# Kernel optimization log

Measured on AMD Instinct MI355X. Metric: run time of the kernel, lower is better.

The kernel has to match this reference:

```python
import jax, jax.numpy as jnp
import numpy as np

VOCAB = 32000
HID = 1024
IN_DIM = 768
LAYERS = 2


def setup_inputs() -> dict:
    key = jax.random.key(0)
    ks = jax.random.split(key, 12)
    s = 0.02
    B, N, S = 8, 16, 512
    return {
        "concepts": jax.random.normal(ks[0], (B, N, IN_DIM), dtype=jnp.float32),
        "target_sequence": jax.random.randint(ks[1], (B, S), 0, VOCAB),
        "embedding": s * jax.random.normal(ks[2], (VOCAB, HID), dtype=jnp.float32),
        "w_ih": s * jax.random.normal(ks[3], (LAYERS, 3 * HID, HID), dtype=jnp.float32),
        "w_hh": s * jax.random.normal(ks[4], (LAYERS, 3 * HID, HID), dtype=jnp.float32),
        "b_ih": jnp.zeros((LAYERS, 3 * HID), dtype=jnp.float32),
        "b_hh": jnp.zeros((LAYERS, 3 * HID), dtype=jnp.float32),
        "fc_w": s * jax.random.normal(ks[5], (VOCAB, HID), dtype=jnp.float32),
        "fc_b": jnp.zeros((VOCAB,), dtype=jnp.float32),
        "c2h_w": s * jax.random.normal(ks[6], (HID * LAYERS, IN_DIM), dtype=jnp.float32),
        "c2h_b": jnp.zeros((HID * LAYERS,), dtype=jnp.float32),
    }


def _gru_layer(x, h0, w_ih, w_hh, b_ih, b_hh):
    # x: [B,S,H], h0: [B,H]. PyTorch GRU gate order: r, z, n.
    xg = jnp.einsum('bsh,gh->bsg', x, w_ih) + b_ih  # precompute input gates [B,S,3H]

    def step(h, xg_t):
        hg = h @ w_hh.T + b_hh
        xr, xz, xn = jnp.split(xg_t, 3, axis=-1)
        hr, hz, hn = jnp.split(hg, 3, axis=-1)
        r = jax.nn.sigmoid(xr + hr)
        z = jax.nn.sigmoid(xz + hz)
        n = jnp.tanh(xn + r * hn)
        h_new = (1.0 - z) * n + z * h
        return h_new, h_new

    _, ys = jax.lax.scan(step, h0, jnp.swapaxes(xg, 0, 1))  # [S,B,H]
    return jnp.swapaxes(ys, 0, 1)


def reference(concepts, target_sequence, embedding, w_ih, w_hh, b_ih, b_hh,
              fc_w, fc_b, c2h_w, c2h_b):
    B = concepts.shape[0]
    global_context = jnp.mean(concepts, axis=1)  # [B, D]
    h0 = (global_context @ c2h_w.T + c2h_b).reshape(B, LAYERS, HID)
    h0 = jnp.swapaxes(h0, 0, 1)  # [L, B, H] matching torch view(L, B, H)
    x = embedding[target_sequence]  # [B, S, H]
    for l in range(LAYERS):
        x = _gru_layer(x, h0[l], w_ih[l], w_hh[l], b_ih[l], b_hh[l])
    logits = jnp.einsum('bsh,vh->bsv', x, fc_w) + fc_b
    return logits
```

## Files before the change

### kernel.cpp

```cpp
#include <hip/hip_runtime.h>
#include <hip/hip_bf16.h>
#include <stdint.h>

#define B_ 8
#define S_ 512
#define H_ 1024
#define V_ 32000
#define D_ 768
#define G3H (3*H_)

typedef __bf16 bf16x8_t __attribute__((ext_vector_type(8)));
typedef float f32x4_t __attribute__((ext_vector_type(4)));

__device__ __forceinline__ unsigned short f2bf(float f) {
  unsigned int u = __float_as_uint(f);
  u += 0x7fffu + ((u >> 16) & 1u);
  return (unsigned short)(u >> 16);
}
__device__ __forceinline__ float fast_sigmoid(float x) {
  float e = __builtin_amdgcn_exp2f(x * -1.44269504088896340736f);
  return __builtin_amdgcn_rcpf(1.0f + e);
}
__device__ __forceinline__ float fast_tanh(float x) {
  float e = __builtin_amdgcn_exp2f(x * -2.88539008177792681472f);
  return 2.0f * __builtin_amdgcn_rcpf(1.0f + e) - 1.0f;
}

__global__ void zero_buf(uint4* __restrict__ p, int n) {
  int i = blockIdx.x * 256 + threadIdx.x;
  if (i < n) p[i] = uint4{0, 0, 0, 0};
}

__global__ void ctx_mean(const float* __restrict__ c, float* __restrict__ ctx) {
  int b = blockIdx.x;
  for (int d = threadIdx.x; d < D_; d += 256) {
    float s = 0.f;
    #pragma unroll
    for (int n = 0; n < 16; ++n) s += c[((size_t)b * 16 + n) * D_ + d];
    ctx[b * D_ + d] = s * (1.0f / 16.0f);
  }
}

__global__ void h0_compute(const float* __restrict__ ctx, const float* __restrict__ w,
                           const float* __restrict__ bias, float* __restrict__ h0l,
                           unsigned short* __restrict__ hb) {
  int o = blockIdx.x * 256 + threadIdx.x;
  int b = o >> 11, row = o & 2047;
  float s = bias[row];
  const float* cw = w + (size_t)row * D_;
  const float* cb = ctx + b * D_;
  for (int d = 0; d < D_; ++d) s += cb[d] * cw[d];
  int layer = row >> 10, u = row & 1023;
  h0l[((size_t)layer * 8 + b) * 1024 + u] = s;
  hb[(size_t)layer * 32768 + b * 1024 + u] = f2bf(s);
}

__global__ void gather_embed(const int* __restrict__ seq, const float* __restrict__ emb,
                             unsigned short* __restrict__ x) {
  int r = blockIdx.x;
  int idx = seq[r];
  float4 v = ((const float4*)(emb + (size_t)idx * H_))[threadIdx.x];
  ushort4 o;
  o.x = f2bf(v.x); o.y = f2bf(v.y); o.z = f2bf(v.z); o.w = f2bf(v.w);
  ((ushort4*)(x + (size_t)r * H_))[threadIdx.x] = o;
}

__global__ void f32_to_bf16(const float* __restrict__ in, unsigned short* __restrict__ outp, long n4) {
  long i = blockIdx.x * (long)blockDim.x + threadIdx.x;
  long stride = (long)gridDim.x * blockDim.x;
  for (; i < n4; i += stride) {
    float4 v = ((const float4*)in)[i];
    ushort4 o;
    o.x = f2bf(v.x); o.y = f2bf(v.y); o.z = f2bf(v.z); o.w = f2bf(v.w);
    ((ushort4*)outp)[i] = o;
  }
}

__global__ __launch_bounds__(256) void gemm_bt_bf16(
    const unsigned short* __restrict__ A, const unsigned short* __restrict__ B,
    float* __restrict__ C, const float* __restrict__ bias,
    int M, int N, int K)
{
  __shared__ __align__(16) unsigned short As[128 * 32];
  __shared__ __align__(16) unsigned short Bs[128 * 32];
  const int tid = threadIdx.x;
  const int l = tid & 63;
  const int w = tid >> 6;
  const int wr = w >> 1, wc = w & 1;
  const long row0 = (long)blockIdx.y * 128;
  const long col0 = (long)blockIdx.x * 128;

  f32x4_t acc[4][4];
  #pragma unroll
  for (int m = 0; m < 4; ++m)
    #pragma unroll
    for (int n = 0; n < 4; ++n) acc[m][n] = (f32x4_t)0.0f;

  const int sr = tid >> 2;
  const int sc = (tid & 3) << 3;

  for (int kt = 0; kt < K; kt += 32) {
    __syncthreads();
    uint4 a0 = *(const uint4*)&A[(row0 + sr) * K + kt + sc];
    uint4 a1 = *(const uint4*)&A[(row0 + sr + 64) * K + kt + sc];
    uint4 b0 = *(const uint4*)&B[(col0 + sr) * K + kt + sc];
    uint4 b1 = *(const uint4*)&B[(col0 + sr + 64) * K + kt + sc];
    ((uint4*)As)[tid]       = a0;
    ((uint4*)As)[tid + 256] = a1;
    ((uint4*)Bs)[tid]       = b0;
    ((uint4*)Bs)[tid + 256] = b1;
    __syncthreads();

    bf16x8_t af[4], bfr[4];
    #pragma unroll
    for (int m = 0; m < 4; ++m)
      af[m] = *(const bf16x8_t*)&As[(wr * 64 + m * 16 + (l & 15)) * 32 + (l >> 4) * 8];
    #pragma unroll
    for (int n = 0; n < 4; ++n)
      bfr[n] = *(const bf16x8_t*)&Bs[(wc * 64 + n * 16 + (l & 15)) * 32 + (l >> 4) * 8];
    #pragma unroll
    for (int m = 0; m < 4; ++m)
      #pragma unroll
      for (int n = 0; n < 4; ++n)
        acc[m][n] = __builtin_amdgcn_mfma_f32_16x16x32_bf16(af[m], bfr[n], acc[m][n], 0, 0, 0);
  }

  #pragma unroll
  for (int n = 0; n < 4; ++n) {
    const long col = col0 + wc * 64 + n * 16 + (l & 15);
    const float bv = bias[col];
    #pragma unroll
    for (int m = 0; m < 4; ++m) {
      const long rbase = row0 + wr * 64 + m * 16 + ((l >> 4) << 2);
      #pragma unroll
      for (int v = 0; v < 4; ++v)
        C[(rbase + v) * (long)N + col] = acc[m][n][v] + bv;
    }
  }
}

__device__ __forceinline__ void load_wfrag(const float* __restrict__ W, int j0, int w,
                                           int l15, int lhi, bf16x8_t wf[2][8]) {
  #pragma unroll
  for (int m = 0; m < 2; ++m) {
    const int idx = m * 16 + l15;
    const int gg = idx >> 3, uu = idx & 7;
    #pragma unroll
    for (int c = 0; c < 8; ++c) {
      f32x4_t v0 = {0.f, 0.f, 0.f, 0.f}, v1 = {0.f, 0.f, 0.f, 0.f};
      if (idx < 24) {
        const float* p = W + (size_t)((gg << 10) + j0 + uu) * 1024
                           + (w << 8) + (c << 5) + (lhi << 3);
        v0 = *(const f32x4_t*)p;
        v1 = *(const f32x4_t*)(p + 4);
      }
      bf16x8_t f;
      f[0] = (__bf16)v0[0]; f[1] = (__bf16)v0[1]; f[2] = (__bf16)v0[2]; f[3] = (__bf16)v0[3];
      f[4] = (__bf16)v1[0]; f[5] = (__bf16)v1[1]; f[6] = (__bf16)v1[2]; f[7] = (__bf16)v1[3];
      wf[m][c] = f;
    }
  }
}

__global__ __launch_bounds__(256, 1) void gru_fused(
    const float* __restrict__ xg,
    const float* __restrict__ w_hh,
    const float* __restrict__ w_ih,
    const float* __restrict__ b_hh,
    const float* __restrict__ b_ih,
    const float* __restrict__ h0f,
    unsigned short* __restrict__ y,
    unsigned short* __restrict__ hb,
    int* __restrict__ flags)
{
  __shared__ __align__(16) float red[4 * 3 * 256];
  const int tid = threadIdx.x;
  const int blk = blockIdx.x;
  const int layer = blk >> 7;
  const int j0 = (blk & 127) * 8;
  const int w = tid >> 6;
  const int l = tid & 63;
  const int l15 = l & 15;
  const int lhi = l >> 4;

  const float* whh = w_hh + (size_t)layer * G3H * H_;
  const float* bhh = b_hh + (size_t)layer * G3H;
  const float* bih = b_ih + (size_t)layer * G3H;

  bf16x8_t wfh[2][8], wfi[2][8];
  #pragma unroll
  for (int m = 0; m < 2; ++m)
    #pragma unroll
    for (int c = 0; c < 8; ++c) wfi[m][c] = (bf16x8_t)(__bf16)0.0f;
  load_wfrag(whh, j0, w, l15, lhi, wfh);
  if (layer == 1) load_wfrag(w_ih + (size_t)G3H * H_, j0, w, l15, lhi, wfi);

  const int u = tid & 7;
  const int b = tid >> 3;
  float g_br = 0.f, g_bz = 0.f, g_bnh = 0.f, g_bni = 0.f, hprev = 0.f;
  const float* xgp = nullptr;
  if (tid < 64) {
    float bhr = bhh[j0 + u], bhz = bhh[1024 + j0 + u], bhn = bhh[2048 + j0 + u];
    if (layer == 0) {
      g_br = bhr; g_bz = bhz; g_bnh = bhn;
      xgp = xg + (size_t)(b * S_) * G3H + j0 + u;
    } else {
      g_br = bhr + bih[j0 + u];
      g_bz = bhz + bih[1024 + j0 + u];
      g_bnh = bhn;
      g_bni = bih[2048 + j0 + u];
    }
    hprev = h0f[(size_t)layer * 8192 + b * 1024 + j0 + u];
  }

  unsigned short* const hb0 = hb;
  unsigned short* const hb1 = hb + 32768;
  const int frag_off = l15 * 1024 + (w << 8) + (lhi << 3);

  for (int e = 0; e <= S_; ++e) {
    const bool active = (layer == 0) ? (e < S_) : (e >= 1);
    const int t = (layer == 0) ? e : (e - 1);

    f32x4_t hv[8], yv[8];
    #pragma unroll
    for (int c = 0; c < 8; ++c) { hv[c] = (f32x4_t)0.0f; yv[c] = (f32x4_t)0.0f; }
    float xr = 0.f, xz = 0.f, xn = 0.f;

    f32x4_t a0h = (f32x4_t)0.0f, a1h = (f32x4_t)0.0f, a1i = (f32x4_t)0.0f;

    if (active) {
      if (layer == 0) {
        const unsigned short* hp0 = hb0 + (e & 1) * 16384 + frag_off;
        #pragma unroll
        for (int c = 0; c < 8; ++c)
          asm volatile("global_load_dwordx4 %0, %1, off offset:%2 sc0 sc1"
                       : "=v"(hv[c]) : "v"(hp0), "i"(c * 64) : "memory");
        if (tid < 64) {
          const float* p = xgp + (size_t)t * G3H;
          xr = p[0]; xz = p[1024]; xn = p[2048];
        }
      } else {
        const unsigned short* yp0 = hb0 + (e & 1) * 16384 + frag_off;
        const unsigned short* hp0 = hb1 + ((e + 1) & 1) * 16384 + frag_off;
        #pragma unroll
        for (int c = 0; c < 8; ++c)
          asm volatile("global_load_dwordx4 %0, %1, off offset:%2 sc0 sc1"
                       : "=v"(yv[c]) : "v"(yp0), "i"(c * 64) : "memory");
        #pragma unroll
        for (int c = 0; c < 8; ++c)
          asm volatile("global_load_dwordx4 %0, %1, off offset:%2 sc0 sc1"
                       : "=v"(hv[c]) : "v"(hp0), "i"(c * 64) : "memory");
      }
      asm volatile("s_waitcnt vmcnt(0)" ::: "memory");
      __builtin_amdgcn_sched_barrier(0);

      #pragma unroll
      for (int c = 0; c < 8; ++c) {
        bf16x8_t hfc = __builtin_bit_cast(bf16x8_t, hv[c]);
        a0h = __builtin_amdgcn_mfma_f32_16x16x32_bf16(wfh[0][c], hfc, a0h, 0, 0, 0);
        a1h = __builtin_amdgcn_mfma_f32_16x16x32_bf16(wfh[1][c], hfc, a1h, 0, 0, 0);
      }
      if (layer == 1) {
        #pragma unroll
        for (int c = 0; c < 8; ++c) {
          bf16x8_t yfc = __builtin_bit_cast(bf16x8_t, yv[c]);
          a0h = __builtin_amdgcn_mfma_f32_16x16x32_bf16(wfi[0][c], yfc, a0h, 0, 0, 0);
          a1i = __builtin_amdgcn_mfma_f32_16x16x32_bf16(wfi[1][c], yfc, a1i, 0, 0, 0);
        }
      }
      *(f32x4_t*)&red[(w * 3 + 0) * 256 + (l << 2)] = a0h;
      *(f32x4_t*)&red[(w * 3 + 1) * 256 + (l << 2)] = a1h;
      *(f32x4_t*)&red[(w * 3 + 2) * 256 + (l << 2)] = a1i;
    }
    __syncthreads();

    if (active && tid < 64) {
      const int base0 = (((u >> 2) << 4 | b) << 2) + (u & 3);
      const int base1 = base0 + 128;
      float aR = 0.f, aZ = 0.f, aNh = 0.f, aNi = 0.f;
      #pragma unroll
      for (int ww = 0; ww < 4; ++ww) {
        aR  += red[ww * 768 + base0];
        aZ  += red[ww * 768 + base1];
        aNh += red[ww * 768 + 256 + base0];
        aNi += red[ww * 768 + 512 + base0];
      }
      float r, z, n;
      if (layer == 0) {
        r = fast_sigmoid(xr + g_br + aR);
        z = fast_sigmoid(xz + g_bz + aZ);
        n = fast_tanh(xn + r * (aNh + g_bnh));
      } else {
        r = fast_sigmoid(aR + g_br);
        z = fast_sigmoid(aZ + g_bz);
        n = fast_tanh(aNi + g_bni + r * (aNh + g_bnh));
      }
      hprev = (1.0f - z) * n + z * hprev;
      unsigned short hv16 = f2bf(hprev);
      unsigned short* hdst = (layer == 0) ? (hb0 + ((e + 1) & 1) * 16384)
                                          : (hb1 + (e & 1) * 16384);
      if (layer == 1)
        y[(((size_t)(b * S_ + t)) << 10) + j0 + u] = hv16;
      asm volatile("global_store_short %0, %1, off sc0 sc1"
                   :: "v"(hdst + b * 1024 + j0 + u), "v"(hv16) : "memory");
    }
    asm volatile("s_waitcnt vmcnt(0)" ::: "memory");
    __syncthreads();
    if (tid == 0)
      __hip_atomic_store(&flags[blk * 32], e + 1,
                         __ATOMIC_RELAXED, __HIP_MEMORY_SCOPE_AGENT);
    while (__hip_atomic_load(&flags[tid * 32],
                             __ATOMIC_RELAXED, __HIP_MEMORY_SCOPE_AGENT) < e + 1)
      __builtin_amdgcn_s_sleep(1);
    __syncthreads();
  }
}

extern "C" void kernel_launch(void* const* d_in, const int* in_sizes, int n_in,
                              void* d_out, int out_size, void* d_ws, size_t ws_size,
                              hipStream_t stream) {
  (void)in_sizes; (void)n_in; (void)out_size; (void)ws_size;
  const float* concepts = (const float*)d_in[0];
  const int*   seq      = (const int*)d_in[1];
  const float* emb      = (const float*)d_in[2];
  const float* w_ih     = (const float*)d_in[3];
  const float* w_hh     = (const float*)d_in[4];
  const float* b_ih     = (const float*)d_in[5];
  const float* b_hh     = (const float*)d_in[6];
  const float* fc_w     = (const float*)d_in[7];
  const float* fc_b     = (const float*)d_in[8];
  const float* c2h_w    = (const float*)d_in[9];
  const float* c2h_b    = (const float*)d_in[10];
  float* out = (float*)d_out;

  char* ws = (char*)d_ws;
  size_t off = 0;
  auto alloc = [&](size_t bytes) {
    char* p = ws + off;
    off += (bytes + 255) & ~(size_t)255;
    return p;
  };
  unsigned short* xy   = (unsigned short*)alloc((size_t)B_ * S_ * H_ * 2);
  float*          xg   = (float*)alloc((size_t)B_ * S_ * G3H * 4);
  unsigned short* wihb = (unsigned short*)alloc((size_t)G3H * H_ * 2);
  unsigned short* fcwb = (unsigned short*)alloc((size_t)V_ * H_ * 2);
  float*          ctx  = (float*)alloc((size_t)B_ * D_ * 4);
  float*          h0l  = (float*)alloc((size_t)2 * B_ * H_ * 4);
  unsigned short* hb   = (unsigned short*)alloc((size_t)2 * 2 * 16 * 1024 * 2);
  int*            flags= (int*)alloc((size_t)256 * 32 * 4);

  zero_buf<<<dim3(40), dim3(256), 0, stream>>>((uint4*)hb, (131072 + 32768) / 16);
  ctx_mean<<<dim3(8), dim3(256), 0, stream>>>(concepts, ctx);
  h0_compute<<<dim3(64), dim3(256), 0, stream>>>(ctx, c2h_w, c2h_b, h0l, hb);
  gather_embed<<<dim3(B_ * S_), dim3(256), 0, stream>>>(seq, emb, xy);
  f32_to_bf16<<<dim3(1024), dim3(256), 0, stream>>>(w_ih, wihb, (long)G3H * H_ / 4);
  f32_to_bf16<<<dim3(2048), dim3(256), 0, stream>>>(fc_w, fcwb, (long)V_ * H_ / 4);

  gemm_bt_bf16<<<dim3(G3H / 128, (B_ * S_) / 128), dim3(256), 0, stream>>>(
      xy, wihb, xg, b_ih, B_ * S_, G3H, H_);

  gru_fused<<<dim3(256), dim3(256), 0, stream>>>(
      xg, w_hh, w_ih, b_hh, b_ih, h0l, xy, hb, flags);

  gemm_bt_bf16<<<dim3(V_ / 128, (B_ * S_) / 128), dim3(256), 0, stream>>>(
      xy, fcwb, out, fc_b, B_ * S_, V_, H_);
}
```

Before: 2.703 ms.

## Replace global barrier with tagged hidden-state words and per-layer ack flags

The per-step grid-wide flag barrier is removed from the fused GRU kernel. Each hidden-state value is now stored as a 32-bit word carrying the bf16 value and a step tag, and consumers poll their own fragments until every tag matches the expected step. Layer 0 waits only on per-block acks from layer 1 before it overwrites the double-buffered state. This cuts the all-to-all barrier latency on the sequential critical path, at the cost of twice the state traffic, spin-polling loads, and added complexity in the memory-ordering logic.

Result: slower. 4.762 ms (+76.2%).

```diff
diff --git a/kernel.cpp b/kernel.cpp
--- a/kernel.cpp
+++ b/kernel.cpp
@@ -43,7 +43,7 @@
 
 __global__ void h0_compute(const float* __restrict__ ctx, const float* __restrict__ w,
                            const float* __restrict__ bias, float* __restrict__ h0l,
-                           unsigned short* __restrict__ hb) {
+                           uint32_t* __restrict__ tagw) {
   int o = blockIdx.x * 256 + threadIdx.x;
   int b = o >> 11, row = o & 2047;
   float s = bias[row];
@@ -52,7 +52,8 @@
   for (int d = 0; d < D_; ++d) s += cb[d] * cw[d];
   int layer = row >> 10, u = row & 1023;
   h0l[((size_t)layer * 8 + b) * 1024 + u] = s;
-  hb[(size_t)layer * 32768 + b * 1024 + u] = f2bf(s);
+  uint32_t tag = (layer == 0) ? 0u : 1u;
+  tagw[(size_t)layer * 16384 + b * 1024 + u] = (tag << 16) | (uint32_t)f2bf(s);
 }
 
 __global__ void gather_embed(const int* __restrict__ seq, const float* __restrict__ emb,
@@ -139,6 +140,53 @@
   }
 }
 
+template<int NCH>
+__device__ __forceinline__ void poll_tagged(const uint32_t* b0, const uint32_t* b1,
+                                            uint32_t tag, uint4 (&q0)[NCH], uint4 (&q1)[NCH]) {
+  #pragma unroll
+  for (int c = 0; c < NCH; ++c) {
+    const uint32_t* p = (c < 8) ? (b0 + c * 32) : (b1 + (c - 8) * 32);
+    asm volatile("global_load_dwordx4 %0, %2, off sc0 sc1\n\t"
+                 "global_load_dwordx4 %1, %2, off offset:16 sc0 sc1"
+                 : "=&v"(q0[c]), "=&v"(q1[c]) : "v"(p) : "memory");
+  }
+  asm volatile("s_waitcnt vmcnt(0)" ::: "memory");
+  while (true) {
+    uint32_t bad = 0;
+    bool st[NCH];
+    #pragma unroll
+    for (int c = 0; c < NCH; ++c) {
+      uint32_t m = (q0[c].x >> 16) ^ tag;
+      m |= (q0[c].y >> 16) ^ tag;  m |= (q0[c].z >> 16) ^ tag;  m |= (q0[c].w >> 16) ^ tag;
+      m |= (q1[c].x >> 16) ^ tag;  m |= (q1[c].y >> 16) ^ tag;
+      m |= (q1[c].z >> 16) ^ tag;  m |= (q1[c].w >> 16) ^ tag;
+      st[c] = (m != 0);
+      bad |= m;
+    }
+    if (bad == 0) break;
+    __builtin_amdgcn_s_sleep(1);
+    #pragma unroll
+    for (int c = 0; c < NCH; ++c) {
+      if (st[c]) {
+        const uint32_t* p = (c < 8) ? (b0 + c * 32) : (b1 + (c - 8) * 32);
+        asm volatile("global_load_dwordx4 %0, %2, off sc0 sc1\n\t"
+                     "global_load_dwordx4 %1, %2, off offset:16 sc0 sc1"
+                     : "=&v"(q0[c]), "=&v"(q1[c]) : "v"(p) : "memory");
+      }
+    }
+    asm volatile("s_waitcnt vmcnt(0)" ::: "memory");
+  }
+}
+
+__device__ __forceinline__ bf16x8_t pack8(const uint4 a, const uint4 b) {
+  uint4 r;
+  r.x = (a.x & 0xFFFFu) | (a.y << 16);
+  r.y = (a.z & 0xFFFFu) | (a.w << 16);
+  r.z = (b.x & 0xFFFFu) | (b.y << 16);
+  r.w = (b.z & 0xFFFFu) | (b.w << 16);
+  return __builtin_bit_cast(bf16x8_t, r);
+}
+
 __device__ __forceinline__ void load_wfrag(const float* __restrict__ W, int j0, int w,
                                            int l15, int lhi, bf16x8_t wf[2][8]) {
   #pragma unroll
@@ -170,8 +218,8 @@
     const float* __restrict__ b_ih,
     const float* __restrict__ h0f,
     unsigned short* __restrict__ y,
-    unsigned short* __restrict__ hb,
-    int* __restrict__ flags)
+    uint32_t* __restrict__ tagw,
+    int* __restrict__ acks)
 {
   __shared__ __align__(16) float red[4 * 3 * 256];
   const int tid = threadIdx.x;
@@ -182,6 +230,7 @@
   const int l = tid & 63;
   const int l15 = l & 15;
   const int lhi = l >> 4;
+  const bool realrow = (l15 < 8);
 
   const float* whh = w_hh + (size_t)layer * G3H * H_;
   const float* bhh = b_hh + (size_t)layer * G3H;
@@ -213,59 +262,63 @@
     hprev = h0f[(size_t)layer * 8192 + b * 1024 + j0 + u];
   }
 
-  unsigned short* const hb0 = hb;
-  unsigned short* const hb1 = hb + 32768;
-  const int frag_off = l15 * 1024 + (w << 8) + (lhi << 3);
+  uint32_t* const tb0 = tagw;
+  uint32_t* const tb1 = tagw + 16384;
+  const int frag_u32 = l15 * 1024 + (w << 8) + (lhi << 3);
+
+  __syncthreads();
 
   for (int e = 0; e <= S_; ++e) {
     const bool active = (layer == 0) ? (e < S_) : (e >= 1);
     const int t = (layer == 0) ? e : (e - 1);
-
-    f32x4_t hv[8], yv[8];
-    #pragma unroll
-    for (int c = 0; c < 8; ++c) { hv[c] = (f32x4_t)0.0f; yv[c] = (f32x4_t)0.0f; }
+    const uint32_t tag = (uint32_t)e;
+
+    if (layer == 0 && active && tid < 128) {
+      while (__hip_atomic_load(&acks[tid], __ATOMIC_RELAXED, __HIP_MEMORY_SCOPE_AGENT) < e - 1)
+        __builtin_amdgcn_s_sleep(1);
+    }
+
     float xr = 0.f, xz = 0.f, xn = 0.f;
-
     f32x4_t a0h = (f32x4_t)0.0f, a1h = (f32x4_t)0.0f, a1i = (f32x4_t)0.0f;
 
     if (active) {
       if (layer == 0) {
-        const unsigned short* hp0 = hb0 + (e & 1) * 16384 + frag_off;
-        #pragma unroll
-        for (int c = 0; c < 8; ++c)
-          asm volatile("global_load_dwordx4 %0, %1, off offset:%2 sc0 sc1"
-                       : "=v"(hv[c]) : "v"(hp0), "i"(c * 64) : "memory");
         if (tid < 64) {
           const float* p = xgp + (size_t)t * G3H;
           xr = p[0]; xz = p[1024]; xn = p[2048];
         }
-      } else {
-        const unsigned short* yp0 = hb0 + (e & 1) * 16384 + frag_off;
-        const unsigned short* hp0 = hb1 + ((e + 1) & 1) * 16384 + frag_off;
+        uint4 q0[8], q1[8];
         #pragma unroll
-        for (int c = 0; c < 8; ++c)
-          asm volatile("global_load_dwordx4 %0, %1, off offset:%2 sc0 sc1"
-                       : "=v"(yv[c]) : "v"(yp0), "i"(c * 64) : "memory");
-        #pragma unroll
-        for (int c = 0; c < 8; ++c)
-          asm volatile("global_load_dwordx4 %0, %1, off offset:%2 sc0 sc1"
-                       : "=v"(hv[c]) : "v"(hp0), "i"(c * 64) : "memory");
-      }
-      asm volatile("s_waitcnt vmcnt(0)" ::: "memory");
-      __builtin_amdgcn_sched_barrier(0);
-
-      #pragma unroll
-      for (int c = 0; c < 8; ++c) {
-        bf16x8_t hfc = __builtin_bit_cast(bf16x8_t, hv[c]);
-        a0h = __builtin_amdgcn_mfma_f32_16x16x32_bf16(wfh[0][c], hfc, a0h, 0, 0, 0);
-        a1h = __builtin_amdgcn_mfma_f32_16x16x32_bf16(wfh[1][c], hfc, a1h, 0, 0, 0);
-      }
-      if (layer == 1) {
+        for (int c = 0; c < 8; ++c) { q0[c] = uint4{0,0,0,0}; q1[c] = uint4{0,0,0,0}; }
+        if (realrow) {
+          const uint32_t* hp = tb0 + (e & 1) * 8192 + frag_u32;
+          poll_tagged<8>(hp, hp, tag, q0, q1);
+        }
+        __builtin_amdgcn_sched_barrier(0);
         #pragma unroll
         for (int c = 0; c < 8; ++c) {
-          bf16x8_t yfc = __builtin_bit_cast(bf16x8_t, yv[c]);
-          a0h = __builtin_amdgcn_mfma_f32_16x16x32_bf16(wfi[0][c], yfc, a0h, 0, 0, 0);
-          a1i = __builtin_amdgcn_mfma_f32_16x16x32_bf16(wfi[1][c], yfc, a1i, 0, 0, 0);
+          bf16x8_t hf = pack8(q0[c], q1[c]);
+          a0h = __builtin_amdgcn_mfma_f32_16x16x32_bf16(wfh[0][c], hf, a0h, 0, 0, 0);
+          a1h = __builtin_amdgcn_mfma_f32_16x16x32_bf16(wfh[1][c], hf, a1h, 0, 0, 0);
+        }
+      } else {
+        uint4 q0[16], q1[16];
+        #pragma unroll
+        for (int c = 0; c < 16; ++c) { q0[c] = uint4{0,0,0,0}; q1[c] = uint4{0,0,0,0}; }
+        if (realrow) {
+          const uint32_t* yp = tb0 + (e & 1) * 8192 + frag_u32;
+          const uint32_t* hp = tb1 + ((e + 1) & 1) * 8192 + frag_u32;
+          poll_tagged<16>(yp, hp, tag, q0, q1);
+        }
+        __builtin_amdgcn_sched_barrier(0);
+        #pragma unroll
+        for (int c = 0; c < 8; ++c) {
+          bf16x8_t yf = pack8(q0[c], q1[c]);
+          bf16x8_t hf = pack8(q0[8 + c], q1[8 + c]);
+          a0h = __builtin_amdgcn_mfma_f32_16x16x32_bf16(wfh[0][c], hf, a0h, 0, 0, 0);
+          a1h = __builtin_amdgcn_mfma_f32_16x16x32_bf16(wfh[1][c], hf, a1h, 0, 0, 0);
+          a0h = __builtin_amdgcn_mfma_f32_16x16x32_bf16(wfi[0][c], yf, a0h, 0, 0, 0);
+          a1i = __builtin_amdgcn_mfma_f32_16x16x32_bf16(wfi[1][c], yf, a1i, 0, 0, 0);
         }
       }
       *(f32x4_t*)&red[(w * 3 + 0) * 256 + (l << 2)] = a0h;
@@ -273,6 +326,9 @@
       *(f32x4_t*)&red[(w * 3 + 2) * 256 + (l << 2)] = a1i;
     }
     __syncthreads();
+
+    if (layer == 1 && active && tid == 0)
+      __hip_atomic_store(&acks[blk & 127], e, __ATOMIC_RELAXED, __HIP_MEMORY_SCOPE_AGENT);
 
     if (active && tid < 64) {
       const int base0 = (((u >> 2) << 4 | b) << 2) + (u & 3);
@@ -297,21 +353,15 @@
       }
       hprev = (1.0f - z) * n + z * hprev;
       unsigned short hv16 = f2bf(hprev);
-      unsigned short* hdst = (layer == 0) ? (hb0 + ((e + 1) & 1) * 16384)
-                                          : (hb1 + (e & 1) * 16384);
+      uint32_t word = ((uint32_t)(e + 1) << 16) | (uint32_t)hv16;
+      uint32_t* hdst = (layer == 0)
+          ? (tb0 + ((e + 1) & 1) * 8192 + b * 1024 + j0 + u)
+          : (tb1 + (e & 1) * 8192 + b * 1024 + j0 + u);
       if (layer == 1)
         y[(((size_t)(b * S_ + t)) << 10) + j0 + u] = hv16;
-      asm volatile("global_store_short %0, %1, off sc0 sc1"
-                   :: "v"(hdst + b * 1024 + j0 + u), "v"(hv16) : "memory");
-    }
-    asm volatile("s_waitcnt vmcnt(0)" ::: "memory");
-    __syncthreads();
-    if (tid == 0)
-      __hip_atomic_store(&flags[blk * 32], e + 1,
-                         __ATOMIC_RELAXED, __HIP_MEMORY_SCOPE_AGENT);
-    while (__hip_atomic_load(&flags[tid * 32],
-                             __ATOMIC_RELAXED, __HIP_MEMORY_SCOPE_AGENT) < e + 1)
-      __builtin_amdgcn_s_sleep(1);
+      asm volatile("global_store_dword %0, %1, off sc0 sc1"
+                   :: "v"(hdst), "v"(word) : "memory");
+    }
     __syncthreads();
   }
 }
@@ -346,12 +396,12 @@
   unsigned short* fcwb = (unsigned short*)alloc((size_t)V_ * H_ * 2);
   float*          ctx  = (float*)alloc((size_t)B_ * D_ * 4);
   float*          h0l  = (float*)alloc((size_t)2 * B_ * H_ * 4);
-  unsigned short* hb   = (unsigned short*)alloc((size_t)2 * 2 * 16 * 1024 * 2);
-  int*            flags= (int*)alloc((size_t)256 * 32 * 4);
-
-  zero_buf<<<dim3(40), dim3(256), 0, stream>>>((uint4*)hb, (131072 + 32768) / 16);
+  uint32_t*       tagw = (uint32_t*)alloc((size_t)2 * 2 * 8 * 1024 * 4);
+  int*            acks = (int*)alloc((size_t)128 * 4);
+
+  zero_buf<<<dim3(1), dim3(256), 0, stream>>>((uint4*)acks, 128 / 4);
   ctx_mean<<<dim3(8), dim3(256), 0, stream>>>(concepts, ctx);
-  h0_compute<<<dim3(64), dim3(256), 0, stream>>>(ctx, c2h_w, c2h_b, h0l, hb);
+  h0_compute<<<dim3(64), dim3(256), 0, stream>>>(ctx, c2h_w, c2h_b, h0l, tagw);
   gather_embed<<<dim3(B_ * S_), dim3(256), 0, stream>>>(seq, emb, xy);
   f32_to_bf16<<<dim3(1024), dim3(256), 0, stream>>>(w_ih, wihb, (long)G3H * H_ / 4);
   f32_to_bf16<<<dim3(2048), dim3(256), 0, stream>>>(fc_w, fcwb, (long)V_ * H_ / 4);
@@ -360,7 +410,7 @@
       xy, wihb, xg, b_ih, B_ * S_, G3H, H_);
 
   gru_fused<<<dim3(256), dim3(256), 0, stream>>>(
-      xg, w_hh, w_ih, b_hh, b_ih, h0l, xy, hb, flags);
+      xg, w_hh, w_ih, b_hh, b_ih, h0l, xy, tagw, acks);
 
   gemm_bt_bf16<<<dim3(V_ / 128, (B_ * S_) / 128), dim3(256), 0, stream>>>(
       xy, fcwb, out, fc_b, B_ * S_, V_, H_);
```

## Halve GRU persistent blocks and replace global barrier with targeted flag waits

Applied to the files above, without the earlier changes.

The persistent GRU kernel now runs on 128 blocks, each owning 16 hidden units with three gate MFMA fragments per wave, instead of 256 blocks with 8 units. The all-to-all barrier at the end of every step is replaced by waits at the start of each step on only the producer flags it depends on. Layer 0 gets a triple-buffered hidden state so it can run one step ahead of layer 1. Hidden-state stores are widened to packed dwords. The aim is to cut per-step barrier latency, at the cost of more register pressure and more MFMA work per block.

New measurement: 2.505 ms. -7.3%, faster.

```diff
diff --git a/kernel.cpp b/kernel.cpp
--- a/kernel.cpp
+++ b/kernel.cpp
@@ -52,7 +52,7 @@
   for (int d = 0; d < D_; ++d) s += cb[d] * cw[d];
   int layer = row >> 10, u = row & 1023;
   h0l[((size_t)layer * 8 + b) * 1024 + u] = s;
-  hb[(size_t)layer * 32768 + b * 1024 + u] = f2bf(s);
+  hb[(layer ? 24576 : 0) + b * 1024 + u] = f2bf(s);
 }
 
 __global__ void gather_embed(const int* __restrict__ seq, const float* __restrict__ emb,
@@ -139,21 +139,15 @@
   }
 }
 
-__device__ __forceinline__ void load_wfrag(const float* __restrict__ W, int j0, int w,
-                                           int l15, int lhi, bf16x8_t wf[2][8]) {
+__device__ __forceinline__ void load_wfrag3(const float* __restrict__ W, int j0, int w,
+                                            int l15, int lhi, bf16x8_t wf[3][8]) {
   #pragma unroll
-  for (int m = 0; m < 2; ++m) {
-    const int idx = m * 16 + l15;
-    const int gg = idx >> 3, uu = idx & 7;
+  for (int m = 0; m < 3; ++m) {
+    const float* pr = W + (size_t)((m << 10) + j0 + l15) * 1024 + (w << 8) + (lhi << 3);
     #pragma unroll
     for (int c = 0; c < 8; ++c) {
-      f32x4_t v0 = {0.f, 0.f, 0.f, 0.f}, v1 = {0.f, 0.f, 0.f, 0.f};
-      if (idx < 24) {
-        const float* p = W + (size_t)((gg << 10) + j0 + uu) * 1024
-                           + (w << 8) + (c << 5) + (lhi << 3);
-        v0 = *(const f32x4_t*)p;
-        v1 = *(const f32x4_t*)(p + 4);
-      }
+      f32x4_t v0 = *(const f32x4_t*)(pr + (c << 5));
+      f32x4_t v1 = *(const f32x4_t*)(pr + (c << 5) + 4);
       bf16x8_t f;
       f[0] = (__bf16)v0[0]; f[1] = (__bf16)v0[1]; f[2] = (__bf16)v0[2]; f[3] = (__bf16)v0[3];
       f[4] = (__bf16)v1[0]; f[5] = (__bf16)v1[1]; f[6] = (__bf16)v1[2]; f[7] = (__bf16)v1[3];
@@ -171,148 +165,169 @@
     const float* __restrict__ h0f,
     unsigned short* __restrict__ y,
     unsigned short* __restrict__ hb,
-    int* __restrict__ flags)
+    int* __restrict__ fl)
 {
-  __shared__ __align__(16) float red[4 * 3 * 256];
+  __shared__ __align__(16) float red[4 * 4 * 256];
   const int tid = threadIdx.x;
   const int blk = blockIdx.x;
-  const int layer = blk >> 7;
-  const int j0 = (blk & 127) * 8;
+  const int layer = blk >> 6;
+  const int j0 = (blk & 63) << 4;
   const int w = tid >> 6;
   const int l = tid & 63;
   const int l15 = l & 15;
   const int lhi = l >> 4;
-
-  const float* whh = w_hh + (size_t)layer * G3H * H_;
-  const float* bhh = b_hh + (size_t)layer * G3H;
-  const float* bih = b_ih + (size_t)layer * G3H;
-
-  bf16x8_t wfh[2][8], wfi[2][8];
+  const bool realrow = (l15 < 8);
+
+  bf16x8_t wfh[3][8], wfi[3][8];
   #pragma unroll
-  for (int m = 0; m < 2; ++m)
+  for (int m = 0; m < 3; ++m)
     #pragma unroll
     for (int c = 0; c < 8; ++c) wfi[m][c] = (bf16x8_t)(__bf16)0.0f;
-  load_wfrag(whh, j0, w, l15, lhi, wfh);
-  if (layer == 1) load_wfrag(w_ih + (size_t)G3H * H_, j0, w, l15, lhi, wfi);
-
-  const int u = tid & 7;
+  load_wfrag3(w_hh + (size_t)layer * G3H * H_, j0, w, l15, lhi, wfh);
+  if (layer == 1) load_wfrag3(w_ih + (size_t)G3H * H_, j0, w, l15, lhi, wfi);
+
+  const int up = tid & 7;
   const int b = tid >> 3;
-  float g_br = 0.f, g_bz = 0.f, g_bnh = 0.f, g_bni = 0.f, hprev = 0.f;
+  float gbr0 = 0.f, gbz0 = 0.f, gbnh0 = 0.f, gbni0 = 0.f, hp0 = 0.f;
+  float gbr1 = 0.f, gbz1 = 0.f, gbnh1 = 0.f, gbni1 = 0.f, hp1 = 0.f;
   const float* xgp = nullptr;
   if (tid < 64) {
-    float bhr = bhh[j0 + u], bhz = bhh[1024 + j0 + u], bhn = bhh[2048 + j0 + u];
+    const float* bhh_l = b_hh + (size_t)layer * G3H;
+    const float* bih_l = b_ih + (size_t)layer * G3H;
+    const int uj = j0 + 2 * up;
+    float bhr0 = bhh_l[uj],     bhz0 = bhh_l[1024 + uj],     bhn0 = bhh_l[2048 + uj];
+    float bhr1 = bhh_l[uj + 1], bhz1 = bhh_l[1024 + uj + 1], bhn1 = bhh_l[2048 + uj + 1];
     if (layer == 0) {
-      g_br = bhr; g_bz = bhz; g_bnh = bhn;
-      xgp = xg + (size_t)(b * S_) * G3H + j0 + u;
+      gbr0 = bhr0; gbz0 = bhz0; gbnh0 = bhn0;
+      gbr1 = bhr1; gbz1 = bhz1; gbnh1 = bhn1;
+      xgp = xg + (size_t)(b * S_) * G3H + uj;
     } else {
-      g_br = bhr + bih[j0 + u];
-      g_bz = bhz + bih[1024 + j0 + u];
-      g_bnh = bhn;
-      g_bni = bih[2048 + j0 + u];
-    }
-    hprev = h0f[(size_t)layer * 8192 + b * 1024 + j0 + u];
+      gbr0 = bhr0 + bih_l[uj];     gbz0 = bhz0 + bih_l[1024 + uj];
+      gbnh0 = bhn0;                gbni0 = bih_l[2048 + uj];
+      gbr1 = bhr1 + bih_l[uj + 1]; gbz1 = bhz1 + bih_l[1024 + uj + 1];
+      gbnh1 = bhn1;                gbni1 = bih_l[2048 + uj + 1];
+    }
+    float2 h2 = *(const float2*)&h0f[(size_t)layer * 8192 + b * 1024 + uj];
+    hp0 = h2.x; hp1 = h2.y;
   }
 
   unsigned short* const hb0 = hb;
-  unsigned short* const hb1 = hb + 32768;
-  const int frag_off = l15 * 1024 + (w << 8) + (lhi << 3);
+  unsigned short* const hb1 = hb + 24576;
+  const int frag = l15 * 1024 + (w << 8) + (lhi << 3);
 
   for (int e = 0; e <= S_; ++e) {
     const bool active = (layer == 0) ? (e < S_) : (e >= 1);
     const int t = (layer == 0) ? e : (e - 1);
-
-    f32x4_t hv[8], yv[8];
-    #pragma unroll
-    for (int c = 0; c < 8; ++c) { hv[c] = (f32x4_t)0.0f; yv[c] = (f32x4_t)0.0f; }
-    float xr = 0.f, xz = 0.f, xn = 0.f;
-
-    f32x4_t a0h = (f32x4_t)0.0f, a1h = (f32x4_t)0.0f, a1i = (f32x4_t)0.0f;
+    const int s3 = e % 3;
+
+    if (tid >= 64 && tid < 192) {
+      const int idx = tid - 64;
+      const int thr = (idx < 64) ? e : ((layer == 0) ? (e - 1) : e);
+      while (__hip_atomic_load(&fl[idx * 32], __ATOMIC_RELAXED, __HIP_MEMORY_SCOPE_AGENT) < thr)
+        __builtin_amdgcn_s_sleep(1);
+    }
+    __syncthreads();
+
+    f32x4_t accR = (f32x4_t)0.0f, accZ = (f32x4_t)0.0f;
+    f32x4_t accNh = (f32x4_t)0.0f, accNi = (f32x4_t)0.0f;
+    float2 xr2 = {0.f, 0.f}, xz2 = {0.f, 0.f}, xn2 = {0.f, 0.f};
 
     if (active) {
-      if (layer == 0) {
-        const unsigned short* hp0 = hb0 + (e & 1) * 16384 + frag_off;
+      f32x4_t hv[8], yv[8];
+      #pragma unroll
+      for (int c = 0; c < 8; ++c) { hv[c] = (f32x4_t)0.0f; yv[c] = (f32x4_t)0.0f; }
+      if (realrow) {
+        const unsigned short* hp = (layer == 0) ? (hb0 + s3 * 8192 + frag)
+                                                : (hb1 + ((e + 1) & 1) * 8192 + frag);
         #pragma unroll
         for (int c = 0; c < 8; ++c)
           asm volatile("global_load_dwordx4 %0, %1, off offset:%2 sc0 sc1"
-                       : "=v"(hv[c]) : "v"(hp0), "i"(c * 64) : "memory");
-        if (tid < 64) {
-          const float* p = xgp + (size_t)t * G3H;
-          xr = p[0]; xz = p[1024]; xn = p[2048];
+                       : "=v"(hv[c]) : "v"(hp), "i"(c * 64) : "memory");
+        if (layer == 1) {
+          const unsigned short* yp = hb0 + s3 * 8192 + frag;
+          #pragma unroll
+          for (int c = 0; c < 8; ++c)
+            asm volatile("global_load_dwordx4 %0, %1, off offset:%2 sc0 sc1"
+                         : "=v"(yv[c]) : "v"(yp), "i"(c * 64) : "memory");
         }
-      } else {
-        const unsigned short* yp0 = hb0 + (e & 1) * 16384 + frag_off;
-        const unsigned short* hp0 = hb1 + ((e + 1) & 1) * 16384 + frag_off;
-        #pragma unroll
-        for (int c = 0; c < 8; ++c)
-          asm volatile("global_load_dwordx4 %0, %1, off offset:%2 sc0 sc1"
-                       : "=v"(yv[c]) : "v"(yp0), "i"(c * 64) : "memory");
-        #pragma unroll
-        for (int c = 0; c < 8; ++c)
-          asm volatile("global_load_dwordx4 %0, %1, off offset:%2 sc0 sc1"
-                       : "=v"(hv[c]) : "v"(hp0), "i"(c * 64) : "memory");
+      }
+      if (layer == 0 && tid < 64) {
+        const float* p = xgp + (size_t)t * G3H;
+        xr2 = *(const float2*)p;
+        xz2 = *(const float2*)(p + 1024);
+        xn2 = *(const float2*)(p + 2048);
       }
       asm volatile("s_waitcnt vmcnt(0)" ::: "memory");
       __builtin_amdgcn_sched_barrier(0);
 
       #pragma unroll
       for (int c = 0; c < 8; ++c) {
-        bf16x8_t hfc = __builtin_bit_cast(bf16x8_t, hv[c]);
-        a0h = __builtin_amdgcn_mfma_f32_16x16x32_bf16(wfh[0][c], hfc, a0h, 0, 0, 0);
-        a1h = __builtin_amdgcn_mfma_f32_16x16x32_bf16(wfh[1][c], hfc, a1h, 0, 0, 0);
+        bf16x8_t hf = __builtin_bit_cast(bf16x8_t, hv[c]);
+        accR  = __builtin_amdgcn_mfma_f32_16x16x32_bf16(wfh[0][c], hf, accR,  0, 0, 0);
+        accZ  = __builtin_amdgcn_mfma_f32_16x16x32_bf16(wfh[1][c], hf, accZ,  0, 0, 0);
+        accNh = __builtin_amdgcn_mfma_f32_16x16x32_bf16(wfh[2][c], hf, accNh, 0, 0, 0);
       }
       if (layer == 1) {
         #pragma unroll
         for (int c = 0; c < 8; ++c) {
-          bf16x8_t yfc = __builtin_bit_cast(bf16x8_t, yv[c]);
-          a0h = __builtin_amdgcn_mfma_f32_16x16x32_bf16(wfi[0][c], yfc, a0h, 0, 0, 0);
-          a1i = __builtin_amdgcn_mfma_f32_16x16x32_bf16(wfi[1][c], yfc, a1i, 0, 0, 0);
+          bf16x8_t yf = __builtin_bit_cast(bf16x8_t, yv[c]);
+          accR  = __builtin_amdgcn_mfma_f32_16x16x32_bf16(wfi[0][c], yf, accR,  0, 0, 0);
+          accZ  = __builtin_amdgcn_mfma_f32_16x16x32_bf16(wfi[1][c], yf, accZ,  0, 0, 0);
+          accNi = __builtin_amdgcn_mfma_f32_16x16x32_bf16(wfi[2][c], yf, accNi, 0, 0, 0);
         }
       }
-      *(f32x4_t*)&red[(w * 3 + 0) * 256 + (l << 2)] = a0h;
-      *(f32x4_t*)&red[(w * 3 + 1) * 256 + (l << 2)] = a1h;
-      *(f32x4_t*)&red[(w * 3 + 2) * 256 + (l << 2)] = a1i;
+      *(f32x4_t*)&red[(w * 4 + 0) * 256 + (l << 2)] = accR;
+      *(f32x4_t*)&red[(w * 4 + 1) * 256 + (l << 2)] = accZ;
+      *(f32x4_t*)&red[(w * 4 + 2) * 256 + (l << 2)] = accNh;
+      *(f32x4_t*)&red[(w * 4 + 3) * 256 + (l << 2)] = accNi;
     }
     __syncthreads();
 
     if (active && tid < 64) {
-      const int base0 = (((u >> 2) << 4 | b) << 2) + (u & 3);
-      const int base1 = base0 + 128;
-      float aR = 0.f, aZ = 0.f, aNh = 0.f, aNi = 0.f;
+      const int u0 = 2 * up, u1 = 2 * up + 1;
+      const int i0 = ((((u0 >> 2) << 4) | b) << 2) + (u0 & 3);
+      const int i1 = ((((u1 >> 2) << 4) | b) << 2) + (u1 & 3);
+      float aR0 = 0.f, aZ0 = 0.f, aNh0 = 0.f, aNi0 = 0.f;
+      float aR1 = 0.f, aZ1 = 0.f, aNh1 = 0.f, aNi1 = 0.f;
       #pragma unroll
       for (int ww = 0; ww < 4; ++ww) {
-        aR  += red[ww * 768 + base0];
-        aZ  += red[ww * 768 + base1];
-        aNh += red[ww * 768 + 256 + base0];
-        aNi += red[ww * 768 + 512 + base0];
-      }
-      float r, z, n;
+        const float* rw = red + ww * 1024;
+        aR0  += rw[i0];        aR1  += rw[i1];
+        aZ0  += rw[256 + i0];  aZ1  += rw[256 + i1];
+        aNh0 += rw[512 + i0];  aNh1 += rw[512 + i1];
+        aNi0 += rw[768 + i0];  aNi1 += rw[768 + i1];
+      }
+      float r0, z0, n0, r1, z1, n1;
       if (layer == 0) {
-        r = fast_sigmoid(xr + g_br + aR);
-        z = fast_sigmoid(xz + g_bz + aZ);
-        n = fast_tanh(xn + r * (aNh + g_bnh));
+        r0 = fast_sigmoid(xr2.x + gbr0 + aR0);
+        z0 = fast_sigmoid(xz2.x + gbz0 + aZ0);
+        n0 = fast_tanh(xn2.x + r0 * (aNh0 + gbnh0));
+        r1 = fast_sigmoid(xr2.y + gbr1 + aR1);
+        z1 = fast_sigmoid(xz2.y + gbz1 + aZ1);
+        n1 = fast_tanh(xn2.y + r1 * (aNh1 + gbnh1));
       } else {
-        r = fast_sigmoid(aR + g_br);
-        z = fast_sigmoid(aZ + g_bz);
-        n = fast_tanh(aNi + g_bni + r * (aNh + g_bnh));
-      }
-      hprev = (1.0f - z) * n + z * hprev;
-      unsigned short hv16 = f2bf(hprev);
-      unsigned short* hdst = (layer == 0) ? (hb0 + ((e + 1) & 1) * 16384)
-                                          : (hb1 + (e & 1) * 16384);
+        r0 = fast_sigmoid(aR0 + gbr0);
+        z0 = fast_sigmoid(aZ0 + gbz0);
+        n0 = fast_tanh(aNi0 + gbni0 + r0 * (aNh0 + gbnh0));
+        r1 = fast_sigmoid(aR1 + gbr1);
+        z1 = fast_sigmoid(aZ1 + gbz1);
+        n1 = fast_tanh(aNi1 + gbni1 + r1 * (aNh1 + gbnh1));
+      }
+      hp0 = (1.0f - z0) * n0 + z0 * hp0;
+      hp1 = (1.0f - z1) * n1 + z1 * hp1;
+      uint32_t word = ((uint32_t)f2bf(hp1) << 16) | (uint32_t)f2bf(hp0);
+      unsigned short* hdst = (layer == 0)
+          ? (hb0 + ((e + 1) % 3) * 8192 + b * 1024 + j0 + 2 * up)
+          : (hb1 + (e & 1) * 8192 + b * 1024 + j0 + 2 * up);
       if (layer == 1)
-        y[(((size_t)(b * S_ + t)) << 10) + j0 + u] = hv16;
-      asm volatile("global_store_short %0, %1, off sc0 sc1"
-                   :: "v"(hdst + b * 1024 + j0 + u), "v"(hv16) : "memory");
+        *(uint32_t*)&y[(((size_t)(b * S_ + t)) << 10) + j0 + 2 * up] = word;
+      asm volatile("global_store_dword %0, %1, off sc0 sc1"
+                   :: "v"(hdst), "v"(word) : "memory");
     }
     asm volatile("s_waitcnt vmcnt(0)" ::: "memory");
-    __syncthreads();
     if (tid == 0)
-      __hip_atomic_store(&flags[blk * 32], e + 1,
+      __hip_atomic_store(&fl[blk * 32], e + 1,
                          __ATOMIC_RELAXED, __HIP_MEMORY_SCOPE_AGENT);
-    while (__hip_atomic_load(&flags[tid * 32],
-                             __ATOMIC_RELAXED, __HIP_MEMORY_SCOPE_AGENT) < e + 1)
-      __builtin_amdgcn_s_sleep(1);
-    __syncthreads();
   }
 }
 
@@ -346,10 +361,10 @@
   unsigned short* fcwb = (unsigned short*)alloc((size_t)V_ * H_ * 2);
   float*          ctx  = (float*)alloc((size_t)B_ * D_ * 4);
   float*          h0l  = (float*)alloc((size_t)2 * B_ * H_ * 4);
-  unsigned short* hb   = (unsigned short*)alloc((size_t)2 * 2 * 16 * 1024 * 2);
-  int*            flags= (int*)alloc((size_t)256 * 32 * 4);
-
-  zero_buf<<<dim3(40), dim3(256), 0, stream>>>((uint4*)hb, (131072 + 32768) / 16);
+  unsigned short* hb   = (unsigned short*)alloc((size_t)5 * 8 * 1024 * 2);
+  int*            fl   = (int*)alloc((size_t)128 * 32 * 4);
+
+  zero_buf<<<dim3(4), dim3(256), 0, stream>>>((uint4*)fl, 128 * 32 / 4);
   ctx_mean<<<dim3(8), dim3(256), 0, stream>>>(concepts, ctx);
   h0_compute<<<dim3(64), dim3(256), 0, stream>>>(ctx, c2h_w, c2h_b, h0l, hb);
   gather_embed<<<dim3(B_ * S_), dim3(256), 0, stream>>>(seq, emb, xy);
@@ -359,8 +374,8 @@
   gemm_bt_bf16<<<dim3(G3H / 128, (B_ * S_) / 128), dim3(256), 0, stream>>>(
       xy, wihb, xg, b_ih, B_ * S_, G3H, H_);
 
-  gru_fused<<<dim3(256), dim3(256), 0, stream>>>(
-      xg, w_hh, w_ih, b_hh, b_ih, h0l, xy, hb, flags);
+  gru_fused<<<dim3(128), dim3(256), 0, stream>>>(
+      xg, w_hh, w_ih, b_hh, b_ih, h0l, xy, hb, fl);
 
   gemm_bt_bf16<<<dim3(V_ / 128, (B_ * S_) / 128), dim3(256), 0, stream>>>(
       xy, fcwb, out, fc_b, B_ * S_, V_, H_);
```
